# Optimization experiments

Hardware: AMD Instinct MI355X
Metric: run time of the kernel (lower is better)

Reference implementation:

```python
import jax, jax.numpy as jnp
import numpy as np

N_EMBD = 768
N_HEAD = 12
HEAD_DIM = N_EMBD // N_HEAD
B, T = 2, 2048
EPS = 1e-5


def setup_inputs() -> dict:
    key = jax.random.key(0)
    ks = jax.random.split(key, 16)
    s = 0.02
    return {
        "x": jax.random.normal(ks[0], (B, T, N_EMBD), dtype=jnp.float32),
        "ln1_g": jnp.ones((N_EMBD,), jnp.float32),
        "ln1_b": jnp.zeros((N_EMBD,), jnp.float32),
        "W_attn": jax.random.normal(ks[1], (N_EMBD, 3 * N_EMBD), jnp.float32) * s,
        "b_attn": jnp.zeros((3 * N_EMBD,), jnp.float32),
        "W_cproj": jax.random.normal(ks[2], (N_EMBD, N_EMBD), jnp.float32) * s,
        "b_cproj": jnp.zeros((N_EMBD,), jnp.float32),
        "ln2_g": jnp.ones((N_EMBD,), jnp.float32),
        "ln2_b": jnp.zeros((N_EMBD,), jnp.float32),
        "W_fc": jax.random.normal(ks[3], (N_EMBD, 4 * N_EMBD), jnp.float32) * s,
        "b_fc": jnp.zeros((4 * N_EMBD,), jnp.float32),
        "W_mproj": jax.random.normal(ks[4], (4 * N_EMBD, N_EMBD), jnp.float32) * s,
        "b_mproj": jnp.zeros((N_EMBD,), jnp.float32),
    }


def _layernorm(x, g, b):
    mu = jnp.mean(x, axis=-1, keepdims=True)
    var = jnp.mean(jnp.square(x - mu), axis=-1, keepdims=True)
    return (x - mu) * jax.lax.rsqrt(var + EPS) * g + b


def _attention(h, W_attn, b_attn, W_cproj, b_cproj):
    Bx, Tx, C = h.shape
    qkv = h @ W_attn + b_attn  # [B, T, 3C]
    q, k, v = jnp.split(qkv, 3, axis=-1)
    # [B, H, T, D]
    def split_heads(t):
        return t.reshape(Bx, Tx, N_HEAD, HEAD_DIM).transpose(0, 2, 1, 3)
    q, k, v = split_heads(q), split_heads(k), split_heads(v)
    att = jnp.einsum("bhqd,bhkd->bhqk", q, k) / np.sqrt(HEAD_DIM).astype(np.float32)
    causal = jnp.tril(jnp.ones((Tx, Tx), dtype=bool))
    att = jnp.where(causal, att, jnp.float32(-jnp.inf))
    att = jax.nn.softmax(att, axis=-1)
    y = jnp.einsum("bhqk,bhkd->bhqd", att, v)
    y = y.transpose(0, 2, 1, 3).reshape(Bx, Tx, C)
    return y @ W_cproj + b_cproj


def _mlp(h, W_fc, b_fc, W_mproj, b_mproj):
    return jax.nn.gelu(h @ W_fc + b_fc, approximate=False) @ W_mproj + b_mproj


def reference(x, ln1_g, ln1_b, W_attn, b_attn, W_cproj, b_cproj,
              ln2_g, ln2_b, W_fc, b_fc, W_mproj, b_mproj):
    x = x + _attention(_layernorm(x, ln1_g, ln1_b), W_attn, b_attn, W_cproj, b_cproj)
    x = x + _mlp(_layernorm(x, ln2_g, ln2_b), W_fc, b_fc, W_mproj, b_mproj)
    return x
```

## Files before the change

kernel.cpp:

```cpp
#include <hip/hip_runtime.h>
#include <cstdint>
#include <cstddef>

#define B_ 2
#define T_ 2048
#define C_ 768
#define H_ 12
#define D_ 64

typedef __attribute__((ext_vector_type(8))) short s16x8;
typedef __attribute__((ext_vector_type(4))) float fx4;

static __device__ __forceinline__ unsigned short f2bf(float f) {
  unsigned u = __builtin_bit_cast(unsigned, f);
  unsigned r = u + 0x7fffu + ((u >> 16) & 1u);
  return (unsigned short)(r >> 16);
}

static __device__ __forceinline__ void glds16(const unsigned short* g, unsigned short* l) {
  __builtin_amdgcn_global_load_lds(
      (const __attribute__((address_space(1))) void*)(g),
      (__attribute__((address_space(3))) void*)(l), 16, 0, 0);
}

__global__ __launch_bounds__(256) void transpose_cast(
    const float* __restrict__ W, unsigned short* __restrict__ Wt, int R, int C) {
  __shared__ float tile[32][33];
  int tx = threadIdx.x & 31;
  int ty = threadIdx.x >> 5;
  int c0 = blockIdx.x * 32, r0 = blockIdx.y * 32;
#pragma unroll
  for (int i = 0; i < 4; ++i)
    tile[ty + i * 8][tx] = W[(size_t)(r0 + ty + i * 8) * C + (c0 + tx)];
  __syncthreads();
#pragma unroll
  for (int i = 0; i < 4; ++i)
    Wt[(size_t)(c0 + ty + i * 8) * R + (r0 + tx)] = f2bf(tile[tx][ty + i * 8]);
}

__global__ __launch_bounds__(256) void layernorm_bf16(
    const float* __restrict__ X, const float* __restrict__ g,
    const float* __restrict__ bb, unsigned short* __restrict__ O) {
  int row = blockIdx.x, tid = threadIdx.x;
  const float* xr = X + (size_t)row * C_;
  float v0 = xr[tid], v1 = xr[tid + 256], v2 = xr[tid + 512];
  float s = v0 + v1 + v2;
  float s2 = v0 * v0 + v1 * v1 + v2 * v2;
#pragma unroll
  for (int off = 1; off < 64; off <<= 1) {
    s += __shfl_xor(s, off);
    s2 += __shfl_xor(s2, off);
  }
  __shared__ float ps[8];
  int wv = tid >> 6;
  if ((tid & 63) == 0) { ps[wv] = s; ps[wv + 4] = s2; }
  __syncthreads();
  s = ps[0] + ps[1] + ps[2] + ps[3];
  s2 = ps[4] + ps[5] + ps[6] + ps[7];
  float mu = s * (1.f / C_);
  float var = s2 * (1.f / C_) - mu * mu;
  float rstd = rsqrtf(var + 1e-5f);
  unsigned short* orow = O + (size_t)row * C_;
  orow[tid]       = f2bf((v0 - mu) * rstd * g[tid]       + bb[tid]);
  orow[tid + 256] = f2bf((v1 - mu) * rstd * g[tid + 256] + bb[tid + 256]);
  orow[tid + 512] = f2bf((v2 - mu) * rstd * g[tid + 512] + bb[tid + 512]);
}

template <int BM, int BN, int BK, int MODE>
__global__ __launch_bounds__(256) void gemm_db(
    const unsigned short* __restrict__ A, const unsigned short* __restrict__ Bt,
    const float* __restrict__ bias, const float* __restrict__ resid,
    float* __restrict__ outF, unsigned short* __restrict__ outB,
    unsigned short* __restrict__ qO, unsigned short* __restrict__ kO,
    unsigned short* __restrict__ vtO, int M, int N, int K) {
  constexpr int AT = BM / 32;
  constexpr int BT = BN / 32;
  constexpr int KS = BK / 32;
  constexpr int CA = BM * BK / 2048;
  constexpr int CB = BN * BK / 2048;
  constexpr int ASZ = BM * BK, BSZ = BN * BK;
  constexpr bool SWIZ = (BK == 64);
  __shared__ __align__(16) unsigned short As[2 * ASZ];
  __shared__ __align__(16) unsigned short Bs[2 * BSZ];
  int tid = threadIdx.x;
  int wv = tid >> 6, lane = tid & 63, quad = lane >> 4, l15 = lane & 15;
  int wm = wv >> 1, wn = wv & 1;
  int m0, n0;
  if (MODE == 1) { m0 = blockIdx.x * BM; n0 = blockIdx.y * BN; }
  else           { n0 = blockIdx.x * BN; m0 = blockIdx.y * BM; }
  fx4 acc[AT][BT];
#pragma unroll
  for (int i = 0; i < AT; ++i)
#pragma unroll
    for (int j = 0; j < BT; ++j) acc[i][j] = fx4{0.f, 0.f, 0.f, 0.f};

  int nk = K / BK;
#pragma unroll
  for (int i = 0; i < CA; ++i) {
    int e = (i * 256 + tid) * 8;
    int row = e / BK, col = e & (BK - 1);
    if (SWIZ) col = (((col >> 3) ^ (row & 7)) << 3);
    glds16(&A[(size_t)(m0 + row) * K + col], &As[(i * 256 + (tid & ~63)) * 8]);
  }
#pragma unroll
  for (int i = 0; i < CB; ++i) {
    int e = (i * 256 + tid) * 8;
    int row = e / BK, col = e & (BK - 1);
    if (SWIZ) col = (((col >> 3) ^ (row & 7)) << 3);
    glds16(&Bt[(size_t)(n0 + row) * K + col], &Bs[(i * 256 + (tid & ~63)) * 8]);
  }
  for (int kt = 0; kt < nk; ++kt) {
    int cur = kt & 1;
    __syncthreads();
    if (kt + 1 < nk) {
      int kb = (kt + 1) * BK;
      int nxt = cur ^ 1;
#pragma unroll
      for (int i = 0; i < CA; ++i) {
        int e = (i * 256 + tid) * 8;
        int row = e / BK, col = e & (BK - 1);
        if (SWIZ) col = (((col >> 3) ^ (row & 7)) << 3);
        glds16(&A[(size_t)(m0 + row) * K + kb + col],
               &As[nxt * ASZ + (i * 256 + (tid & ~63)) * 8]);
      }
#pragma unroll
      for (int i = 0; i < CB; ++i) {
        int e = (i * 256 + tid) * 8;
        int row = e / BK, col = e & (BK - 1);
        if (SWIZ) col = (((col >> 3) ^ (row & 7)) << 3);
        glds16(&Bt[(size_t)(n0 + row) * K + kb + col],
               &Bs[nxt * BSZ + (i * 256 + (tid & ~63)) * 8]);
      }
    }
#pragma unroll
    for (int ks = 0; ks < KS; ++ks) {
      s16x8 af[AT], bf[BT];
#pragma unroll
      for (int mt = 0; mt < AT; ++mt) {
        int r = wm * (BM / 2) + mt * 16 + l15;
        int c = ks * 32 + quad * 8;
        if (SWIZ) c = (((c >> 3) ^ (r & 7)) << 3);
        af[mt] = *(const s16x8*)&As[cur * ASZ + r * BK + c];
      }
#pragma unroll
      for (int nt = 0; nt < BT; ++nt) {
        int r = wn * (BN / 2) + nt * 16 + l15;
        int c = ks * 32 + quad * 8;
        if (SWIZ) c = (((c >> 3) ^ (r & 7)) << 3);
        bf[nt] = *(const s16x8*)&Bs[cur * BSZ + r * BK + c];
      }
#pragma unroll
      for (int mt = 0; mt < AT; ++mt)
#pragma unroll
        for (int nt = 0; nt < BT; ++nt)
          acc[mt][nt] = __builtin_amdgcn_mfma_f32_16x16x32_bf16(af[mt], bf[nt], acc[mt][nt], 0, 0, 0);
    }
  }

#pragma unroll
  for (int mt = 0; mt < AT; ++mt)
#pragma unroll
    for (int nt = 0; nt < BT; ++nt)
#pragma unroll
      for (int r = 0; r < 4; ++r) {
        int m = m0 + wm * (BM / 2) + mt * 16 + quad * 4 + r;
        int n = n0 + wn * (BN / 2) + nt * 16 + l15;
        float v = acc[mt][nt][r] + bias[n];
        if (MODE == 0) {
          int which = n / C_;
          int within = n - which * C_;
          int hd = within >> 6, d = within & 63;
          int bbx = m >> 11, t = m & 2047;
          size_t bh = (size_t)(bbx * H_ + hd);
          unsigned short bv = f2bf(v);
          if (which == 0)      qO[(bh * T_ + t) * D_ + d] = bv;
          else if (which == 1) kO[(bh * T_ + t) * D_ + d] = bv;
          else                 vtO[(bh * D_ + d) * T_ + t] = bv;
        } else if (MODE == 1) {
          outF[(size_t)m * N + n] = resid[(size_t)m * N + n] + v;
        } else {
          float gl = 0.5f * v * (1.f + erff(v * 0.70710678118654752f));
          outB[(size_t)m * N + n] = f2bf(gl);
        }
      }
}

__global__ __launch_bounds__(256) void attn_fused(
    const unsigned short* __restrict__ Q, const unsigned short* __restrict__ Kg,
    const unsigned short* __restrict__ Vt, unsigned short* __restrict__ Y) {
  __shared__ __align__(16) unsigned short Ks[64 * 72];
  __shared__ __align__(16) unsigned short Vs[64 * 72];
  __shared__ __align__(16) unsigned short Ps[4][16 * 72];
  int tid = threadIdx.x;
  int wv = tid >> 6, lane = tid & 63, quad = lane >> 4, l15 = lane & 15;
  int l = blockIdx.x;
  int w = l >> 8, s = l & 255;
  int g = s >> 5, i = s & 31;
  int qt, bh;
  if (w == 0)      { qt = i;              bh = g; }
  else if (w == 1) { qt = 31 - i;         bh = 8 + g; }
  else             { qt = (i + 16) & 31;  bh = 16 + g; }
  int bbx = bh / H_, hh = bh - bbx * H_;
  int q0 = qt * 64;
  size_t base = (size_t)bh * T_ * D_;
  size_t vbase = (size_t)bh * D_ * T_;
  int qrow = q0 + wv * 16 + l15;
  s16x8 qf0 = *(const s16x8*)&Q[base + (size_t)qrow * D_ + quad * 8];
  s16x8 qf1 = *(const s16x8*)&Q[base + (size_t)qrow * D_ + 32 + quad * 8];
  float lsum[4];
  fx4 oacc[4];
#pragma unroll
  for (int t = 0; t < 4; ++t) {
    lsum[t] = 0.f;
    oacc[t] = fx4{0.f, 0.f, 0.f, 0.f};
  }
  int r0s = tid >> 3;
  int c8 = (tid & 7) * 8;
  uint4 ka, kc, va, vc;
  {
    ka = *(const uint4*)&Kg[base + (size_t)r0s * D_ + c8];
    kc = *(const uint4*)&Kg[base + (size_t)(r0s + 32) * D_ + c8];
    va = *(const uint4*)&Vt[vbase + (size_t)r0s * T_ + c8];
    vc = *(const uint4*)&Vt[vbase + (size_t)(r0s + 32) * T_ + c8];
  }
  for (int kb = 0; kb <= qt; ++kb) {
    int k0 = kb * 64;
    __syncthreads();
    *(uint4*)&Ks[r0s * 72 + c8] = ka;
    *(uint4*)&Ks[(r0s + 32) * 72 + c8] = kc;
    *(uint4*)&Vs[r0s * 72 + c8] = va;
    *(uint4*)&Vs[(r0s + 32) * 72 + c8] = vc;
    __syncthreads();
    if (kb < qt) {
      int kn = k0 + 64;
      ka = *(const uint4*)&Kg[base + (size_t)(kn + r0s) * D_ + c8];
      kc = *(const uint4*)&Kg[base + (size_t)(kn + r0s + 32) * D_ + c8];
      va = *(const uint4*)&Vt[vbase + (size_t)r0s * T_ + kn + c8];
      vc = *(const uint4*)&Vt[vbase + (size_t)(r0s + 32) * T_ + kn + c8];
    }
    fx4 sc[4];
#pragma unroll
    for (int nt = 0; nt < 4; ++nt) {
      sc[nt] = fx4{0.f, 0.f, 0.f, 0.f};
      s16x8 kf0 = *(const s16x8*)&Ks[(nt * 16 + l15) * 72 + quad * 8];
      s16x8 kf1 = *(const s16x8*)&Ks[(nt * 16 + l15) * 72 + 32 + quad * 8];
      sc[nt] = __builtin_amdgcn_mfma_f32_16x16x32_bf16(qf0, kf0, sc[nt], 0, 0, 0);
      sc[nt] = __builtin_amdgcn_mfma_f32_16x16x32_bf16(qf1, kf1, sc[nt], 0, 0, 0);
    }
    bool diag = (kb == qt);
    unsigned short* pw = &Ps[wv][0];
#pragma unroll
    for (int nt = 0; nt < 4; ++nt)
#pragma unroll
      for (int r = 0; r < 4; ++r) {
        float p;
        if (diag && (k0 + nt * 16 + l15) > (q0 + wv * 16 + quad * 4 + r)) {
          p = 0.f;
        } else {
          p = __expf(sc[nt][r] * 0.125f);
        }
        lsum[r] += p;
        pw[(quad * 4 + r) * 72 + nt * 16 + l15] = f2bf(p);
      }
    s16x8 pa0 = *(const s16x8*)&pw[l15 * 72 + quad * 8];
    s16x8 pa1 = *(const s16x8*)&pw[l15 * 72 + 32 + quad * 8];
#pragma unroll
    for (int nt = 0; nt < 4; ++nt) {
      s16x8 vf0 = *(const s16x8*)&Vs[(nt * 16 + l15) * 72 + quad * 8];
      s16x8 vf1 = *(const s16x8*)&Vs[(nt * 16 + l15) * 72 + 32 + quad * 8];
      oacc[nt] = __builtin_amdgcn_mfma_f32_16x16x32_bf16(pa0, vf0, oacc[nt], 0, 0, 0);
      oacc[nt] = __builtin_amdgcn_mfma_f32_16x16x32_bf16(pa1, vf1, oacc[nt], 0, 0, 0);
    }
  }
#pragma unroll
  for (int r = 0; r < 4; ++r) {
#pragma unroll
    for (int off = 1; off < 16; off <<= 1) lsum[r] += __shfl_xor(lsum[r], off);
  }
#pragma unroll
  for (int nt = 0; nt < 4; ++nt)
#pragma unroll
    for (int r = 0; r < 4; ++r) {
      float o = oacc[nt][r] / lsum[r];
      int token = bbx * T_ + q0 + wv * 16 + quad * 4 + r;
      Y[(size_t)token * C_ + hh * D_ + nt * 16 + l15] = f2bf(o);
    }
}

extern "C" void kernel_launch(void* const* d_in, const int* in_sizes, int n_in,
                              void* d_out, int out_size, void* d_ws, size_t ws_size,
                              hipStream_t stream) {
  const float* x      = (const float*)d_in[0];
  const float* ln1g   = (const float*)d_in[1];
  const float* ln1b   = (const float*)d_in[2];
  const float* Wattn  = (const float*)d_in[3];
  const float* battn  = (const float*)d_in[4];
  const float* Wcproj = (const float*)d_in[5];
  const float* bcproj = (const float*)d_in[6];
  const float* ln2g   = (const float*)d_in[7];
  const float* ln2b   = (const float*)d_in[8];
  const float* Wfc    = (const float*)d_in[9];
  const float* bfc    = (const float*)d_in[10];
  const float* Wmproj = (const float*)d_in[11];
  const float* bmproj = (const float*)d_in[12];
  float* out = (float*)d_out;
  char* ws = (char*)d_ws;

  unsigned short* WattnT  = (unsigned short*)(ws + 0);
  unsigned short* WcprojT = (unsigned short*)(ws + 3538944);
  unsigned short* WfcT    = (unsigned short*)(ws + 4718592);
  unsigned short* WmprojT = (unsigned short*)(ws + 9437184);
  unsigned short* hbuf    = (unsigned short*)(ws + 14155776);
  unsigned short* Qb      = (unsigned short*)(ws + 20447232);
  unsigned short* Kb      = (unsigned short*)(ws + 26738688);
  unsigned short* Vtb     = (unsigned short*)(ws + 33030144);
  unsigned short* Yb      = (unsigned short*)(ws + 39321600);
  float*          x1      = (float*)(ws + 45613056);
  unsigned short* Ab      = (unsigned short*)(ws + 58195968);

  transpose_cast<<<dim3(2304 / 32, 768 / 32), 256, 0, stream>>>(Wattn, WattnT, 768, 2304);
  transpose_cast<<<dim3(768 / 32, 768 / 32), 256, 0, stream>>>(Wcproj, WcprojT, 768, 768);
  transpose_cast<<<dim3(3072 / 32, 768 / 32), 256, 0, stream>>>(Wfc, WfcT, 768, 3072);
  transpose_cast<<<dim3(768 / 32, 3072 / 32), 256, 0, stream>>>(Wmproj, WmprojT, 3072, 768);

  layernorm_bf16<<<4096, 256, 0, stream>>>(x, ln1g, ln1b, hbuf);

  gemm_db<128, 128, 32, 0><<<dim3(2304 / 128, 4096 / 128), 256, 0, stream>>>(
      hbuf, WattnT, battn, nullptr, nullptr, nullptr, Qb, Kb, Vtb, 4096, 2304, 768);

  attn_fused<<<768, 256, 0, stream>>>(Qb, Kb, Vtb, Yb);

  gemm_db<128, 64, 64, 1><<<dim3(4096 / 128, 768 / 64), 256, 0, stream>>>(
      Yb, WcprojT, bcproj, x, x1, nullptr, nullptr, nullptr, nullptr, 4096, 768, 768);

  layernorm_bf16<<<4096, 256, 0, stream>>>(x1, ln2g, ln2b, hbuf);

  gemm_db<128, 128, 32, 2><<<dim3(3072 / 128, 4096 / 128), 256, 0, stream>>>(
      hbuf, WfcT, bfc, nullptr, nullptr, Ab, nullptr, nullptr, nullptr, 4096, 3072, 768);

  gemm_db<128, 64, 64, 1><<<dim3(4096 / 128, 768 / 64), 256, 0, stream>>>(
      Ab, WmprojT, bmproj, x1, out, nullptr, nullptr, nullptr, nullptr, 4096, 768, 3072);
}
```

Before: 291.1 us.

## Vectorize V-transpose epilogue stores, reorder attention tile schedule, truncate P to bf16

The QKV GEMM epilogue now packs the four consecutive-t values for the transposed V output into a single 8-byte store, where it previously issued four scattered 2-byte stores. The attention block-to-(head, q-tile) mapping is changed to a different interleaving of causal tile sizes, meant to balance work across blocks. The softmax probabilities are converted to bf16 by truncation rather than round-to-nearest, saving a few ALU ops per element at the cost of a small downward rounding bias.

```diff
diff --git a/kernel.cpp b/kernel.cpp
--- a/kernel.cpp
+++ b/kernel.cpp
@@ -15,6 +15,9 @@
   unsigned u = __builtin_bit_cast(unsigned, f);
   unsigned r = u + 0x7fffu + ((u >> 16) & 1u);
   return (unsigned short)(r >> 16);
+}
+static __device__ __forceinline__ unsigned short f2bf_trunc(float f) {
+  return (unsigned short)(__builtin_bit_cast(unsigned, f) >> 16);
 }
 
 static __device__ __forceinline__ void glds16(const unsigned short* g, unsigned short* l) {
@@ -160,29 +163,45 @@
 #pragma unroll
   for (int mt = 0; mt < AT; ++mt)
 #pragma unroll
-    for (int nt = 0; nt < BT; ++nt)
-#pragma unroll
-      for (int r = 0; r < 4; ++r) {
-        int m = m0 + wm * (BM / 2) + mt * 16 + quad * 4 + r;
-        int n = n0 + wn * (BN / 2) + nt * 16 + l15;
-        float v = acc[mt][nt][r] + bias[n];
-        if (MODE == 0) {
-          int which = n / C_;
-          int within = n - which * C_;
-          int hd = within >> 6, d = within & 63;
-          int bbx = m >> 11, t = m & 2047;
-          size_t bh = (size_t)(bbx * H_ + hd);
-          unsigned short bv = f2bf(v);
-          if (which == 0)      qO[(bh * T_ + t) * D_ + d] = bv;
-          else if (which == 1) kO[(bh * T_ + t) * D_ + d] = bv;
-          else                 vtO[(bh * D_ + d) * T_ + t] = bv;
-        } else if (MODE == 1) {
+    for (int nt = 0; nt < BT; ++nt) {
+      int mb = m0 + wm * (BM / 2) + mt * 16 + quad * 4;
+      int n = n0 + wn * (BN / 2) + nt * 16 + l15;
+      if (MODE == 0) {
+        int which = n / C_;
+        int within = n - which * C_;
+        int hd = within >> 6, d = within & 63;
+        int bbx = mb >> 11, t = mb & 2047;
+        size_t bh = (size_t)(bbx * H_ + hd);
+        float b = bias[n];
+        if (which == 2) {
+          unsigned v01 = (unsigned)f2bf(acc[mt][nt][0] + b) |
+                         ((unsigned)f2bf(acc[mt][nt][1] + b) << 16);
+          unsigned v23 = (unsigned)f2bf(acc[mt][nt][2] + b) |
+                         ((unsigned)f2bf(acc[mt][nt][3] + b) << 16);
+          *(uint2*)&vtO[(bh * D_ + d) * T_ + t] = uint2{v01, v23};
+        } else {
+          unsigned short* dst = (which == 0) ? qO : kO;
+#pragma unroll
+          for (int r = 0; r < 4; ++r)
+            dst[(bh * T_ + t + r) * D_ + d] = f2bf(acc[mt][nt][r] + b);
+        }
+      } else if (MODE == 1) {
+#pragma unroll
+        for (int r = 0; r < 4; ++r) {
+          int m = mb + r;
+          float v = acc[mt][nt][r] + bias[n];
           outF[(size_t)m * N + n] = resid[(size_t)m * N + n] + v;
-        } else {
+        }
+      } else {
+#pragma unroll
+        for (int r = 0; r < 4; ++r) {
+          int m = mb + r;
+          float v = acc[mt][nt][r] + bias[n];
           float gl = 0.5f * v * (1.f + erff(v * 0.70710678118654752f));
           outB[(size_t)m * N + n] = f2bf(gl);
         }
       }
+    }
 }
 
 __global__ __launch_bounds__(256) void attn_fused(
@@ -194,12 +213,13 @@
   int tid = threadIdx.x;
   int wv = tid >> 6, lane = tid & 63, quad = lane >> 4, l15 = lane & 15;
   int l = blockIdx.x;
-  int w = l >> 8, s = l & 255;
-  int g = s >> 5, i = s & 31;
-  int qt, bh;
-  if (w == 0)      { qt = i;              bh = g; }
-  else if (w == 1) { qt = 31 - i;         bh = 8 + g; }
-  else             { qt = (i + 16) & 31;  bh = 16 + g; }
+  int w = l >> 8, c = l & 255;
+  int i = c & 31;
+  int bh = w * 8 + (c >> 5);
+  int qt;
+  if (w == 0)      qt = i;
+  else if (w == 1) qt = (i + 16) & 31;
+  else             qt = (i < 16) ? (30 - 2 * i) : (63 - 2 * i);
   int bbx = bh / H_, hh = bh - bbx * H_;
   int q0 = qt * 64;
   size_t base = (size_t)bh * T_ * D_;
@@ -260,7 +280,7 @@
           p = __expf(sc[nt][r] * 0.125f);
         }
         lsum[r] += p;
-        pw[(quad * 4 + r) * 72 + nt * 16 + l15] = f2bf(p);
+        pw[(quad * 4 + r) * 72 + nt * 16 + l15] = f2bf_trunc(p);
       }
     s16x8 pa0 = *(const s16x8*)&pw[l15 * 72 + quad * 8];
     s16x8 pa1 = *(const s16x8*)&pw[l15 * 72 + 32 + quad * 8];
```

Result: faster. 272.1 us (-6.5%).
